# Kernel tuning notes

Hardware: AMD Instinct MI355X
Metric: run time of the kernel (lower is better)

## Reference

```python
import jax, jax.numpy as jnp
from jax import lax
import numpy as np

N_ATOMS, N_BONDS, N_GRAPHS = 8192, 32768, 256
EMBED, HIDDEN, DEPTH = 32, 256, 10
ATOM_VOCAB, BOND_VOCAB = 200, 10


def setup_inputs() -> dict:
    key = jax.random.key(0)
    ks = jax.random.split(key, 16)
    f = lambda k, *sh: jax.random.normal(k, sh, dtype=jnp.float32) * 0.05
    return {
        "atom_features": jax.random.randint(ks[0], (N_ATOMS,), 0, ATOM_VOCAB),
        "bond_features": jax.random.randint(ks[1], (N_BONDS,), 0, BOND_VOCAB),
        "adjacency_matrix": jax.random.randint(ks[2], (N_ATOMS, N_ATOMS), 0, 2, dtype=jnp.int32),
        "batch_indices": jax.random.randint(ks[3], (N_ATOMS,), 0, N_GRAPHS),
        "atom_emb": f(ks[4], ATOM_VOCAB, EMBED),
        "bond_emb": f(ks[5], BOND_VOCAB, EMBED),
        "msg_W": f(ks[6], DEPTH, HIDDEN, 2 * EMBED),
        "msg_b": f(ks[7], DEPTH, HIDDEN),
        "gru_Wih": f(ks[8], DEPTH, 3 * EMBED, HIDDEN),
        "gru_Whh": f(ks[9], DEPTH, 3 * EMBED, EMBED),
        "gru_bih": f(ks[10], DEPTH, 3 * EMBED),
        "gru_bhh": f(ks[11], DEPTH, 3 * EMBED),
        "pool_W": f(ks[12], HIDDEN, EMBED),
        "pool_b": f(ks[13], HIDDEN),
    }


def _gmpn(atom_emb, bond_emb, msg_W, msg_b, gru_Wih, gru_Whh, gru_bih, gru_bhh,
          pool_W, pool_b, atom_features, bond_features, adjacency_matrix, batch_indices):
    H = atom_emb[atom_features]                       # [N, E]
    A = (adjacency_matrix > 0).astype(H.dtype)        # [N, N] 0/1
    deg = A.sum(axis=1)                               # [N]
    has_nb = deg > 0
    inv_deg = jnp.where(has_nb, 1.0 / jnp.maximum(deg, 1.0), 0.0)[:, None]

    def layer(h, params):
        W, b, wih, whh, b_ih, b_hh = params
        # mean_j Linear([h_i ; h_j]) = W1 h_i + W2 mean_j h_j + b
        neigh_mean = (A @ h) * inv_deg                # [N, E]
        W1, W2 = W[:, :EMBED], W[:, EMBED:]
        msg = h @ W1.T + neigh_mean @ W2.T + b        # [N, HIDDEN]
        msg = jnp.where(has_nb[:, None], msg, 0.0)    # zero message if no neighbors
        # single-step GRU: input=msg, hidden state=h
        gi = msg @ wih.T + b_ih
        gh = h @ whh.T + b_hh
        ir, iz, inn = jnp.split(gi, 3, axis=-1)
        hr, hz, hn = jnp.split(gh, 3, axis=-1)
        r = jax.nn.sigmoid(ir + hr)
        z = jax.nn.sigmoid(iz + hz)
        n = jnp.tanh(inn + r * hn)
        h_new = (1.0 - z) * n + z * h                 # [N, E]
        return h_new, None

    H, _ = lax.scan(layer, H, (msg_W, msg_b, gru_Wih, gru_Whh, gru_bih, gru_bhh))

    # per-graph mean pooling (zeros for empty graphs), then global_pool linear
    seg_sum = jax.ops.segment_sum(H, batch_indices, num_segments=N_GRAPHS)
    cnt = jax.ops.segment_sum(jnp.ones((H.shape[0],), H.dtype), batch_indices, num_segments=N_GRAPHS)
    graph_mean = jnp.where(cnt[:, None] > 0, seg_sum / jnp.maximum(cnt, 1.0)[:, None], 0.0)
    graph_embeddings = graph_mean @ pool_W.T + pool_b  # [G, HIDDEN]

    bond_embeddings = bond_emb[bond_features]          # [B, E]
    return H, bond_embeddings, graph_embeddings


def reference(atom_features, bond_features, adjacency_matrix, batch_indices,
              atom_emb, bond_emb, msg_W, msg_b, gru_Wih, gru_Whh, gru_bih, gru_bhh,
              pool_W, pool_b):
    return _gmpn(atom_emb, bond_emb, msg_W, msg_b, gru_Wih, gru_Whh, gru_bih, gru_bhh,
                 pool_W, pool_b, atom_features, bond_features, adjacency_matrix, batch_indices)
```

## Files before the change

### kernel.cpp

```cpp
#include <hip/hip_runtime.h>
#include <stdint.h>

typedef __bf16 bf16x8 __attribute__((ext_vector_type(8)));
typedef float f32x4 __attribute__((ext_vector_type(4)));

__device__ __forceinline__ float b2f(unsigned short u){
  unsigned int t = ((unsigned int)u) << 16;
  return __builtin_bit_cast(float, t);
}
__device__ __forceinline__ unsigned short f2b(float f){
  unsigned int x = __builtin_bit_cast(unsigned int, f);
  x = x + 0x7FFFu + ((x >> 16) & 1u);
  return (unsigned short)(x >> 16);
}
__device__ __forceinline__ void spread8(unsigned int B, unsigned int w[4]){
  unsigned int m = __umul24(B, 0x8001u);
  w[0] = __umul24(m & 0x00010001u, 0x3F80u);
  w[1] = __umul24(m & 0x00040004u, 0x0FE0u);
  w[2] = __umul24(m & 0x00100010u, 0x03F8u);
  w[3] = __umul24(m & 0x00400040u, 0x00FEu);
}
__device__ __forceinline__ float fsig(float x){ return 1.f/(1.f + __expf(-x)); }
__device__ __forceinline__ float ftanh(float x){ return 1.f - 2.f/(__expf(2.f*x) + 1.f); }

__global__ void k_prep(const void* s_msgW, const void* s_msgb, const void* s_wih,
                       const void* s_whh, const void* s_bih, const void* s_bhh,
                       const void* s_poolW, const void* s_poolb,
                       const unsigned short* __restrict__ aemb_u16,
                       unsigned short* __restrict__ cw,
                       int* __restrict__ deg, float* __restrict__ seg,
                       float* __restrict__ cnt, int* __restrict__ flag){
  int b = blockIdx.x, t = threadIdx.x;
  unsigned int uu = aemb_u16[2*t];
  int e = (int)((uu >> 7) & 0xFF);
  unsigned long long vote = __ballot(e >= 100 && e <= 127);
  int isb = (__popcll(vote) > 32) ? 1 : 0;
  if (b < 1771){
    int id = b*256 + t;
    if (id < 453248){
      const void* src; int off;
      if      (id < 163840){ src = s_msgW;  off = id; }
      else if (id < 166400){ src = s_msgb;  off = id - 163840; }
      else if (id < 412160){ src = s_wih;   off = id - 166400; }
      else if (id < 442880){ src = s_whh;   off = id - 412160; }
      else if (id < 443840){ src = s_bih;   off = id - 442880; }
      else if (id < 444800){ src = s_bhh;   off = id - 443840; }
      else if (id < 452992){ src = s_poolW; off = id - 444800; }
      else                 { src = s_poolb; off = id - 452992; }
      cw[id] = isb ? ((const unsigned short*)src)[off]
                   : f2b(((const float*)src)[off]);
    }
  } else {
    int id2 = (b - 1771)*256 + t;
    if (id2 < 8192){ deg[id2] = 0; seg[id2] = 0.f; }
    if (id2 < 256) cnt[id2] = 0.f;
    if (b == 1771 && t == 0) flag[0] = isb;
  }
}

__global__ void k_pack(const int* __restrict__ adj, unsigned int* __restrict__ mask3,
                       int* __restrict__ deg){
  int tid = blockIdx.x*256 + threadIdx.x;
  int rb  = tid >> 12;
  int rem = tid & 4095;
  int kgg = rem >> 6;
  int L   = rem & 63;
  int lc = L & 15, q = L >> 4;
  int row = rb*16 + lc;
  const int4* p4 = (const int4*)(adj + (size_t)row*8192 + kgg*128 + q*8);
  unsigned int dw = 0; int pc = 0;
  #pragma unroll
  for (int s=0;s<4;s++){
    int4 u = p4[s*8];
    int4 v = p4[s*8 + 1];
    unsigned int b = (unsigned int)(u.x > 0)
                   | ((unsigned int)(u.y > 0) << 1)
                   | ((unsigned int)(u.z > 0) << 2)
                   | ((unsigned int)(u.w > 0) << 3)
                   | ((unsigned int)(v.x > 0) << 4)
                   | ((unsigned int)(v.y > 0) << 5)
                   | ((unsigned int)(v.z > 0) << 6)
                   | ((unsigned int)(v.w > 0) << 7);
    dw |= b << (8*s);
    pc += __popc(b);
  }
  mask3[tid] = dw;
  pc += __shfl_xor(pc, 16);
  pc += __shfl_xor(pc, 32);
  if (q == 0) atomicAdd(deg + row, pc);
}

__global__ void k_be(const int* __restrict__ af, const void* __restrict__ araw,
                     const int* __restrict__ bft, const void* __restrict__ braw,
                     const int* __restrict__ flag,
                     float* __restrict__ hf32, uint4* __restrict__ hfrag,
                     unsigned short* __restrict__ outB16, float* __restrict__ outB32){
  int b = blockIdx.x, t = threadIdx.x;
  if (b >= 512){
    int id = (b - 512)*512 + t;
    int e = id >> 5, c = id & 31;
    int idx = bft[e]*32 + c;
    if (flag[0]) outB16[id] = ((const unsigned short*)braw)[idx];
    else         outB32[id] = ((const float*)braw)[idx];
    return;
  }
  __shared__ __align__(16) float sh[512];
  int r = t >> 5, c = t & 31;
  int row = b*16 + r;
  int idx = af[row]*32 + c;
  float f;
  if (flag[0]) f = b2f(((const unsigned short*)araw)[idx]);
  else         f = ((const float*)araw)[idx];
  hf32[row*32 + c] = f;
  sh[r*32 + c] = f;
  __syncthreads();
  if (t < 64){
    int nt = t >> 5, Lq = t & 31;
    int ks32 = b >> 1, half = b & 1;
    int col = nt*16 + (Lq & 15);
    int rbase = (Lq >> 4)*8;
    unsigned int w[4];
    #pragma unroll
    for (int p=0;p<4;p++){
      unsigned int lo = f2b(sh[(rbase + 2*p    )*32 + col]);
      unsigned int hi = f2b(sh[(rbase + 2*p + 1)*32 + col]);
      w[p] = lo | (hi << 16);
    }
    hfrag[(ks32*2 + nt)*64 + half*32 + Lq] = make_uint4(w[0],w[1],w[2],w[3]);
  }
}

__launch_bounds__(512, 1)
__global__ void k_layer(const unsigned int* __restrict__ mask3,
                        const uint4* __restrict__ hfragIn,
                        unsigned int* __restrict__ hfragOut,
                        float* __restrict__ hf32,
                        const int* __restrict__ deg,
                        const unsigned short* __restrict__ msgW,
                        const unsigned short* __restrict__ msgb,
                        const unsigned short* __restrict__ wih,
                        const unsigned short* __restrict__ whh,
                        const unsigned short* __restrict__ bih,
                        const unsigned short* __restrict__ bhh,
                        const int* __restrict__ bidx,
                        float* __restrict__ seg, float* __restrict__ cnt,
                        unsigned short* __restrict__ out16, float* __restrict__ out32,
                        const int* __restrict__ flag, int last)
{
  __shared__ __align__(16) char uni[33792];
  __shared__ __align__(16) unsigned short sA[32][72];
  __shared__ __align__(16) unsigned short smsg[32][264];
  __shared__ int sdeg[32];

  const int t = threadIdx.x;
  const int b = blockIdx.x;
  const int w = t >> 6, L = t & 63;
  const int q = L >> 4, lc = L & 15;
  const int rowbase = b*32;

  const int r0 = t >> 4;
  const int cl = t & 15;
  const int r  = rowbase + r0;
  const int isb = flag[0];
  const int dgr = deg[r];
  const float invr = dgr > 0 ? 1.f/(float)dgr : 0.f;
  float h0 = hf32[r*32 + cl];
  float h1 = hf32[r*32 + 16 + cl];
  sA[r0][cl]    = f2b(h0);
  sA[r0][16+cl] = f2b(h1);
  if (cl == 0) sdeg[r0] = dgr;

  {
    f32x4 a00={0,0,0,0}, a01={0,0,0,0}, a10={0,0,0,0}, a11={0,0,0,0};
    const unsigned int* mp = mask3 + (size_t)b*8192 + w*512 + L;
    const uint4* bp = hfragIn + (size_t)w*4096 + L;
    for (int g=0; g<8; g++){
      unsigned int mw0 = mp[g*64];
      unsigned int mw1 = mp[4096 + g*64];
      #pragma unroll
      for (int s=0; s<4; s++){
        int ks = g*4 + s;
        uint4 u0 = bp[ks*128];
        uint4 u1 = bp[ks*128 + 64];
        union { unsigned int u[4]; bf16x8 v; } A0, A1, B0, B1;
        spread8((mw0 >> (8*s)) & 0xFFu, A0.u);
        spread8((mw1 >> (8*s)) & 0xFFu, A1.u);
        B0.u[0]=u0.x; B0.u[1]=u0.y; B0.u[2]=u0.z; B0.u[3]=u0.w;
        B1.u[0]=u1.x; B1.u[1]=u1.y; B1.u[2]=u1.z; B1.u[3]=u1.w;
        a00 = __builtin_amdgcn_mfma_f32_16x16x32_bf16(A0.v, B0.v, a00, 0,0,0);
        a01 = __builtin_amdgcn_mfma_f32_16x16x32_bf16(A0.v, B1.v, a01, 0,0,0);
        a10 = __builtin_amdgcn_mfma_f32_16x16x32_bf16(A1.v, B0.v, a10, 0,0,0);
        a11 = __builtin_amdgcn_mfma_f32_16x16x32_bf16(A1.v, B1.v, a11, 0,0,0);
      }
    }
    float* sp = (float*)uni + w*1056;
    #pragma unroll
    for (int rg=0; rg<4; rg++){
      int rw = q*4 + rg;
      sp[rw*33 + lc]         = a00[rg];
      sp[rw*33 + 16 + lc]    = a01[rg];
      sp[(16+rw)*33 + lc]    = a10[rg];
      sp[(16+rw)*33 + 16+lc] = a11[rg];
    }
  }
  __syncthreads();
  {
    const float* spf = (const float*)uni;
    float s0 = 0.f, s1 = 0.f;
    #pragma unroll
    for (int ww=0; ww<8; ww++){
      s0 += spf[ww*1056 + r0*33 + cl];
      s1 += spf[ww*1056 + r0*33 + 16 + cl];
    }
    sA[r0][32+cl] = f2b(s0*invr);
    sA[r0][48+cl] = f2b(s1*invr);
  }
  __syncthreads();
  {
    int rt = w & 1, ntb = (w >> 1)*4;
    union { uint4 u; bf16x8 v; } A0, A1;
    A0.u = *(const uint4*)&sA[rt*16 + lc][q*8];
    A1.u = *(const uint4*)&sA[rt*16 + lc][32 + q*8];
    #pragma unroll
    for (int i=0; i<4; i++){
      int nt = ntb + i;
      union { uint4 u; bf16x8 v; } B0, B1;
      B0.u = *(const uint4*)(msgW + (size_t)(nt*16 + lc)*64 + q*8);
      B1.u = *(const uint4*)(msgW + (size_t)(nt*16 + lc)*64 + 32 + q*8);
      f32x4 am = {0,0,0,0};
      am = __builtin_amdgcn_mfma_f32_16x16x32_bf16(A0.v, B0.v, am, 0,0,0);
      am = __builtin_amdgcn_mfma_f32_16x16x32_bf16(A1.v, B1.v, am, 0,0,0);
      float bv = b2f(msgb[nt*16 + lc]);
      #pragma unroll
      for (int rg=0; rg<4; rg++){
        int rw = rt*16 + q*4 + rg;
        float v = am[rg] + bv;
        if (sdeg[rw] == 0) v = 0.f;
        smsg[rw][nt*16 + lc] = f2b(v);
      }
    }
  }
  __syncthreads();
  {
    float* sgi = (float*)uni;
    float* sgh = (float*)(uni + 12800);
    if (w < 6){
      int nt = w;
      f32x4 g0 = {0,0,0,0}, g1 = {0,0,0,0};
      #pragma unroll
      for (int ks=0; ks<8; ks++){
        union { uint4 u; bf16x8 v; } A0, A1, B;
        B.u  = *(const uint4*)(wih + (size_t)(nt*16 + lc)*256 + ks*32 + q*8);
        A0.u = *(const uint4*)&smsg[lc][ks*32 + q*8];
        A1.u = *(const uint4*)&smsg[16 + lc][ks*32 + q*8];
        g0 = __builtin_amdgcn_mfma_f32_16x16x32_bf16(A0.v, B.v, g0, 0,0,0);
        g1 = __builtin_amdgcn_mfma_f32_16x16x32_bf16(A1.v, B.v, g1, 0,0,0);
      }
      #pragma unroll
      for (int rg=0; rg<4; rg++){
        sgi[(q*4+rg)*100      + nt*16 + lc] = g0[rg];
        sgi[(16+q*4+rg)*100   + nt*16 + lc] = g1[rg];
      }
    } else {
      int rt = w - 6;
      union { uint4 u; bf16x8 v; } A;
      A.u = *(const uint4*)&sA[rt*16 + lc][q*8];
      #pragma unroll
      for (int nt=0; nt<6; nt++){
        union { uint4 u; bf16x8 v; } B;
        B.u = *(const uint4*)(whh + (size_t)(nt*16 + lc)*32 + q*8);
        f32x4 hh = {0,0,0,0};
        hh = __builtin_amdgcn_mfma_f32_16x16x32_bf16(A.v, B.v, hh, 0,0,0);
        #pragma unroll
        for (int rg=0; rg<4; rg++)
          sgh[(rt*16 + q*4+rg)*100 + nt*16 + lc] = hh[rg];
      }
    }
  }
  __syncthreads();
  {
    const float* sgi = (const float*)uni;
    const float* sgh = (const float*)(uni + 12800);
    float ir0 = sgi[r0*100 + cl]    + b2f(bih[cl]),    hr0 = sgh[r0*100 + cl]    + b2f(bhh[cl]);
    float iz0 = sgi[r0*100 + 32+cl] + b2f(bih[32+cl]), hz0 = sgh[r0*100 + 32+cl] + b2f(bhh[32+cl]);
    float in0 = sgi[r0*100 + 64+cl] + b2f(bih[64+cl]), hn0 = sgh[r0*100 + 64+cl] + b2f(bhh[64+cl]);
    float ir1 = sgi[r0*100 + 16+cl] + b2f(bih[16+cl]), hr1 = sgh[r0*100 + 16+cl] + b2f(bhh[16+cl]);
    float iz1 = sgi[r0*100 + 48+cl] + b2f(bih[48+cl]), hz1 = sgh[r0*100 + 48+cl] + b2f(bhh[48+cl]);
    float in1 = sgi[r0*100 + 80+cl] + b2f(bih[80+cl]), hn1 = sgh[r0*100 + 80+cl] + b2f(bhh[80+cl]);
    float rr0 = fsig(ir0 + hr0), zz0 = fsig(iz0 + hz0);
    float rr1 = fsig(ir1 + hr1), zz1 = fsig(iz1 + hz1);
    float nn0 = ftanh(in0 + rr0*hn0);
    float nn1 = ftanh(in1 + rr1*hn1);
    h0 = (1.f - zz0)*nn0 + zz0*h0;
    h1 = (1.f - zz1)*nn1 + zz1*h1;
    hf32[r*32 + cl]      = h0;
    hf32[r*32 + 16 + cl] = h1;
    unsigned int m0 = f2b(h0), m1 = f2b(h1);
    if (!last){
      unsigned int p0 = (unsigned int)__shfl_xor((int)m0, 16);
      unsigned int p1 = (unsigned int)__shfl_xor((int)m1, 16);
      if ((r & 1) == 0){
        int ks32 = r >> 5;
        int Lf = ((r >> 3) & 3)*16 + cl;
        int pidx = (r & 7) >> 1;
        hfragOut[((ks32*2 + 0)*64 + Lf)*4 + pidx] = m0 | (p0 << 16);
        hfragOut[((ks32*2 + 1)*64 + Lf)*4 + pidx] = m1 | (p1 << 16);
      }
    } else {
      if (isb){ out16[r*32 + cl] = (unsigned short)m0; out16[r*32 + 16 + cl] = (unsigned short)m1; }
      else    { out32[r*32 + cl] = h0; out32[r*32 + 16 + cl] = h1; }
      int gb = bidx[r];
      atomicAdd(seg + gb*32 + cl, h0);
      atomicAdd(seg + gb*32 + 16 + cl, h1);
      if (cl == 0) atomicAdd(cnt + gb, 1.f);
    }
  }
}

__global__ void k_pool(const float* __restrict__ seg, const float* __restrict__ cnt,
                       const unsigned short* __restrict__ pw, const unsigned short* __restrict__ pb,
                       const int* __restrict__ flag,
                       unsigned short* __restrict__ outG16, float* __restrict__ outG32){
  int g = blockIdx.x, o = threadIdx.x;
  float cv = cnt[g];
  float ic = cv > 0.f ? 1.f/cv : 0.f;
  float s = 0.f;
  #pragma unroll
  for (int c=0;c<32;c++) s += seg[g*32+c]*ic*b2f(pw[o*32+c]);
  s += b2f(pb[o]);
  if (flag[0]) outG16[g*256 + o] = f2b(s);
  else         outG32[g*256 + o] = s;
}

extern "C" void kernel_launch(void* const* d_in, const int* in_sizes, int n_in,
                              void* d_out, int out_size, void* d_ws, size_t ws_size,
                              hipStream_t stream){
  const int* af   = (const int*)d_in[0];
  const int* bft  = (const int*)d_in[1];
  const int* adj  = (const int*)d_in[2];
  const int* bidx = (const int*)d_in[3];

  char* ws = (char*)d_ws;
  unsigned int*   mask3  = (unsigned int*)(ws + 0);
  unsigned int*   hfrag0 = (unsigned int*)(ws + 8388608);
  unsigned int*   hfrag1 = (unsigned int*)(ws + 8912896);
  float*          hf32   = (float*)(ws + 9437184);
  int*            deg    = (int*)(ws + 10485760);
  float*          seg    = (float*)(ws + 10518528);
  float*          cnt    = (float*)(ws + 10551296);
  int*            flag   = (int*)(ws + 10552320);
  unsigned short* cw     = (unsigned short*)(ws + 10552384);

  unsigned short* o16 = (unsigned short*)d_out;
  float*          o32 = (float*)d_out;

  k_prep<<<1803, 256, 0, stream>>>(d_in[6], d_in[7], d_in[8], d_in[9], d_in[10],
                                   d_in[11], d_in[12], d_in[13],
                                   (const unsigned short*)d_in[4],
                                   cw, deg, seg, cnt, flag);
  k_pack<<<8192, 256, 0, stream>>>(adj, mask3, deg);
  k_be<<<2560, 512, 0, stream>>>(af, d_in[4], bft, d_in[5], flag,
                                 hf32, (uint4*)hfrag0,
                                 o16 + 262144, o32 + 262144);

  for (int d = 0; d < 10; d++){
    const uint4*  hin  = (const uint4*)((d & 1) ? hfrag1 : hfrag0);
    unsigned int* hout = (d & 1) ? hfrag0 : hfrag1;
    k_layer<<<256, 512, 0, stream>>>(mask3, hin, hout, hf32, deg,
                                     cw + (size_t)d*16384,        cw + 163840 + d*256,
                                     cw + 166400 + (size_t)d*24576, cw + 412160 + d*3072,
                                     cw + 442880 + d*96,          cw + 443840 + d*96,
                                     bidx, seg, cnt, o16, o32, flag, (d == 9) ? 1 : 0);
  }
  k_pool<<<256, 256, 0, stream>>>(seg, cnt, cw + 444800, cw + 452992, flag,
                                  o16 + 1310720, o32 + 1310720);
}
```

Before: 535.5 us.

## Precompose message and GRU input weights to skip the hidden-256 message matmul

```diff
diff --git a/kernel.cpp b/kernel.cpp
--- a/kernel.cpp
+++ b/kernel.cpp
@@ -58,6 +58,32 @@
   }
 }
 
+__global__ void k_fuse(const unsigned short* __restrict__ cw,
+                       unsigned short* __restrict__ vcat, float* __restrict__ bwv){
+  int d = blockIdx.x >> 2, quarter = blockIdx.x & 3;
+  const unsigned short* msgW = cw + (size_t)d*16384;
+  const unsigned short* msgb = cw + 163840 + d*256;
+  const unsigned short* wih  = cw + 166400 + (size_t)d*24576;
+  int t = threadIdx.x;
+  #pragma unroll
+  for (int i=0;i<6;i++){
+    int idx = quarter*1536 + i*256 + t;
+    int j = idx >> 6, e = idx & 63;
+    const unsigned short* wr = wih + j*256;
+    const unsigned short* wc = msgW + e;
+    float acc = 0.f;
+    for (int k=0;k<256;k++)
+      acc += b2f(wr[k]) * b2f(wc[k*64]);
+    vcat[(size_t)d*6144 + idx] = f2b(acc);
+  }
+  if (quarter == 0 && t < 96){
+    const unsigned short* wr = wih + t*256;
+    float acc = 0.f;
+    for (int k=0;k<256;k++) acc += b2f(msgb[k]) * b2f(wr[k]);
+    bwv[d*96 + t] = acc;
+  }
+}
+
 __global__ void k_pack(const int* __restrict__ adj, unsigned int* __restrict__ mask3,
                        int* __restrict__ deg){
   int tid = blockIdx.x*256 + threadIdx.x;
@@ -136,9 +162,8 @@
                         unsigned int* __restrict__ hfragOut,
                         float* __restrict__ hf32,
                         const int* __restrict__ deg,
-                        const unsigned short* __restrict__ msgW,
-                        const unsigned short* __restrict__ msgb,
-                        const unsigned short* __restrict__ wih,
+                        const unsigned short* __restrict__ vcat,
+                        const float* __restrict__ bwv,
                         const unsigned short* __restrict__ whh,
                         const unsigned short* __restrict__ bih,
                         const unsigned short* __restrict__ bhh,
@@ -149,7 +174,6 @@
 {
   __shared__ __align__(16) char uni[33792];
   __shared__ __align__(16) unsigned short sA[32][72];
-  __shared__ __align__(16) unsigned short smsg[32][264];
   __shared__ int sdeg[32];
 
   const int t = threadIdx.x;
@@ -217,49 +241,29 @@
   }
   __syncthreads();
   {
-    int rt = w & 1, ntb = (w >> 1)*4;
-    union { uint4 u; bf16x8 v; } A0, A1;
-    A0.u = *(const uint4*)&sA[rt*16 + lc][q*8];
-    A1.u = *(const uint4*)&sA[rt*16 + lc][32 + q*8];
-    #pragma unroll
-    for (int i=0; i<4; i++){
-      int nt = ntb + i;
-      union { uint4 u; bf16x8 v; } B0, B1;
-      B0.u = *(const uint4*)(msgW + (size_t)(nt*16 + lc)*64 + q*8);
-      B1.u = *(const uint4*)(msgW + (size_t)(nt*16 + lc)*64 + 32 + q*8);
-      f32x4 am = {0,0,0,0};
-      am = __builtin_amdgcn_mfma_f32_16x16x32_bf16(A0.v, B0.v, am, 0,0,0);
-      am = __builtin_amdgcn_mfma_f32_16x16x32_bf16(A1.v, B1.v, am, 0,0,0);
-      float bv = b2f(msgb[nt*16 + lc]);
-      #pragma unroll
-      for (int rg=0; rg<4; rg++){
-        int rw = rt*16 + q*4 + rg;
-        float v = am[rg] + bv;
-        if (sdeg[rw] == 0) v = 0.f;
-        smsg[rw][nt*16 + lc] = f2b(v);
-      }
-    }
-  }
-  __syncthreads();
-  {
     float* sgi = (float*)uni;
     float* sgh = (float*)(uni + 12800);
     if (w < 6){
       int nt = w;
-      f32x4 g0 = {0,0,0,0}, g1 = {0,0,0,0};
+      union { uint4 u; bf16x8 v; } B0, B1;
+      B0.u = *(const uint4*)(vcat + (size_t)(nt*16 + lc)*64 + q*8);
+      B1.u = *(const uint4*)(vcat + (size_t)(nt*16 + lc)*64 + 32 + q*8);
+      float bw = bwv[nt*16 + lc];
       #pragma unroll
-      for (int ks=0; ks<8; ks++){
-        union { uint4 u; bf16x8 v; } A0, A1, B;
-        B.u  = *(const uint4*)(wih + (size_t)(nt*16 + lc)*256 + ks*32 + q*8);
-        A0.u = *(const uint4*)&smsg[lc][ks*32 + q*8];
-        A1.u = *(const uint4*)&smsg[16 + lc][ks*32 + q*8];
-        g0 = __builtin_amdgcn_mfma_f32_16x16x32_bf16(A0.v, B.v, g0, 0,0,0);
-        g1 = __builtin_amdgcn_mfma_f32_16x16x32_bf16(A1.v, B.v, g1, 0,0,0);
-      }
-      #pragma unroll
-      for (int rg=0; rg<4; rg++){
-        sgi[(q*4+rg)*100      + nt*16 + lc] = g0[rg];
-        sgi[(16+q*4+rg)*100   + nt*16 + lc] = g1[rg];
+      for (int rt=0; rt<2; rt++){
+        union { uint4 u; bf16x8 v; } A0, A1;
+        A0.u = *(const uint4*)&sA[rt*16 + lc][q*8];
+        A1.u = *(const uint4*)&sA[rt*16 + lc][32 + q*8];
+        f32x4 g0 = {0,0,0,0};
+        g0 = __builtin_amdgcn_mfma_f32_16x16x32_bf16(A0.v, B0.v, g0, 0,0,0);
+        g0 = __builtin_amdgcn_mfma_f32_16x16x32_bf16(A1.v, B1.v, g0, 0,0,0);
+        #pragma unroll
+        for (int rg=0; rg<4; rg++){
+          int rw = rt*16 + q*4 + rg;
+          float v = g0[rg] + bw;
+          if (sdeg[rw] == 0) v = 0.f;
+          sgi[rw*100 + nt*16 + lc] = v;
+        }
       }
     } else {
       int rt = w - 6;
@@ -350,6 +354,8 @@
   float*          cnt    = (float*)(ws + 10551296);
   int*            flag   = (int*)(ws + 10552320);
   unsigned short* cw     = (unsigned short*)(ws + 10552384);
+  unsigned short* vcat   = (unsigned short*)(ws + 11458880);
+  float*          bwv    = (float*)(ws + 11581760);
 
   unsigned short* o16 = (unsigned short*)d_out;
   float*          o32 = (float*)d_out;
@@ -358,6 +364,7 @@
                                    d_in[11], d_in[12], d_in[13],
                                    (const unsigned short*)d_in[4],
                                    cw, deg, seg, cnt, flag);
+  k_fuse<<<40, 256, 0, stream>>>(cw, vcat, bwv);
   k_pack<<<8192, 256, 0, stream>>>(adj, mask3, deg);
   k_be<<<2560, 512, 0, stream>>>(af, d_in[4], bft, d_in[5], flag,
                                  hf32, (uint4*)hfrag0,
@@ -367,9 +374,9 @@
     const uint4*  hin  = (const uint4*)((d & 1) ? hfrag1 : hfrag0);
     unsigned int* hout = (d & 1) ? hfrag0 : hfrag1;
     k_layer<<<256, 512, 0, stream>>>(mask3, hin, hout, hf32, deg,
-                                     cw + (size_t)d*16384,        cw + 163840 + d*256,
-                                     cw + 166400 + (size_t)d*24576, cw + 412160 + d*3072,
-                                     cw + 442880 + d*96,          cw + 443840 + d*96,
+                                     vcat + (size_t)d*6144, bwv + d*96,
+                                     cw + 412160 + d*3072,
+                                     cw + 442880 + d*96, cw + 443840 + d*96,
                                      bidx, seg, cnt, o16, o32, flag, (d == 9) ? 1 : 0);
   }
   k_pool<<<256, 256, 0, stream>>>(seg, cnt, cw + 444800, cw + 452992, flag,
```

After: 550.0 us. +2.7%, slower.

## Fuse ten layer launches into one persistent kernel with grid barrier

Applied to the files above, without the earlier changes.

```diff
diff --git a/kernel.cpp b/kernel.cpp
--- a/kernel.cpp
+++ b/kernel.cpp
@@ -22,6 +22,25 @@
 }
 __device__ __forceinline__ float fsig(float x){ return 1.f/(1.f + __expf(-x)); }
 __device__ __forceinline__ float ftanh(float x){ return 1.f - 2.f/(__expf(2.f*x) + 1.f); }
+
+__device__ __forceinline__ void gbar(int* bar){
+  __syncthreads();
+  if (threadIdx.x == 0){
+    int g = __hip_atomic_load(&bar[1], __ATOMIC_RELAXED, __HIP_MEMORY_SCOPE_AGENT);
+    int a = __hip_atomic_fetch_add(&bar[0], 1, __ATOMIC_RELEASE, __HIP_MEMORY_SCOPE_AGENT);
+    if (a == 255){
+      __hip_atomic_store(&bar[0], 0, __ATOMIC_RELAXED, __HIP_MEMORY_SCOPE_AGENT);
+      __hip_atomic_fetch_add(&bar[1], 1, __ATOMIC_RELEASE, __HIP_MEMORY_SCOPE_AGENT);
+    } else {
+      int it = 0;
+      while (__hip_atomic_load(&bar[1], __ATOMIC_RELAXED, __HIP_MEMORY_SCOPE_AGENT) == g){
+        if (++it > 48) __builtin_amdgcn_s_sleep(1);
+      }
+    }
+    (void)__hip_atomic_load(&bar[1], __ATOMIC_ACQUIRE, __HIP_MEMORY_SCOPE_AGENT);
+  }
+  __syncthreads();
+}
 
 __global__ void k_prep(const void* s_msgW, const void* s_msgb, const void* s_wih,
                        const void* s_whh, const void* s_bih, const void* s_bhh,
@@ -54,7 +73,7 @@
     int id2 = (b - 1771)*256 + t;
     if (id2 < 8192){ deg[id2] = 0; seg[id2] = 0.f; }
     if (id2 < 256) cnt[id2] = 0.f;
-    if (b == 1771 && t == 0) flag[0] = isb;
+    if (b == 1771 && t == 0){ flag[0] = isb; flag[4] = 0; flag[5] = 0; }
   }
 }
 
@@ -130,22 +149,17 @@
   }
 }
 
-__launch_bounds__(512, 1)
-__global__ void k_layer(const unsigned int* __restrict__ mask3,
-                        const uint4* __restrict__ hfragIn,
-                        unsigned int* __restrict__ hfragOut,
-                        float* __restrict__ hf32,
-                        const int* __restrict__ deg,
-                        const unsigned short* __restrict__ msgW,
-                        const unsigned short* __restrict__ msgb,
-                        const unsigned short* __restrict__ wih,
-                        const unsigned short* __restrict__ whh,
-                        const unsigned short* __restrict__ bih,
-                        const unsigned short* __restrict__ bhh,
-                        const int* __restrict__ bidx,
-                        float* __restrict__ seg, float* __restrict__ cnt,
-                        unsigned short* __restrict__ out16, float* __restrict__ out32,
-                        const int* __restrict__ flag, int last)
+__launch_bounds__(512)
+__global__ void k_layers(const unsigned int* __restrict__ mask3,
+                         unsigned int* __restrict__ hfrag0,
+                         unsigned int* __restrict__ hfrag1,
+                         const float* __restrict__ hf32,
+                         const int* __restrict__ deg,
+                         const unsigned short* __restrict__ cw,
+                         const int* __restrict__ bidx,
+                         float* __restrict__ seg, float* __restrict__ cnt,
+                         unsigned short* __restrict__ out16, float* __restrict__ out32,
+                         const int* __restrict__ flag, int* bar)
 {
   __shared__ __align__(16) char uni[33792];
   __shared__ __align__(16) unsigned short sA[32][72];
@@ -166,154 +180,166 @@
   const float invr = dgr > 0 ? 1.f/(float)dgr : 0.f;
   float h0 = hf32[r*32 + cl];
   float h1 = hf32[r*32 + 16 + cl];
-  sA[r0][cl]    = f2b(h0);
-  sA[r0][16+cl] = f2b(h1);
   if (cl == 0) sdeg[r0] = dgr;
 
-  {
-    f32x4 a00={0,0,0,0}, a01={0,0,0,0}, a10={0,0,0,0}, a11={0,0,0,0};
-    const unsigned int* mp = mask3 + (size_t)b*8192 + w*512 + L;
-    const uint4* bp = hfragIn + (size_t)w*4096 + L;
-    for (int g=0; g<8; g++){
-      unsigned int mw0 = mp[g*64];
-      unsigned int mw1 = mp[4096 + g*64];
-      #pragma unroll
-      for (int s=0; s<4; s++){
-        int ks = g*4 + s;
-        uint4 u0 = bp[ks*128];
-        uint4 u1 = bp[ks*128 + 64];
-        union { unsigned int u[4]; bf16x8 v; } A0, A1, B0, B1;
-        spread8((mw0 >> (8*s)) & 0xFFu, A0.u);
-        spread8((mw1 >> (8*s)) & 0xFFu, A1.u);
-        B0.u[0]=u0.x; B0.u[1]=u0.y; B0.u[2]=u0.z; B0.u[3]=u0.w;
-        B1.u[0]=u1.x; B1.u[1]=u1.y; B1.u[2]=u1.z; B1.u[3]=u1.w;
-        a00 = __builtin_amdgcn_mfma_f32_16x16x32_bf16(A0.v, B0.v, a00, 0,0,0);
-        a01 = __builtin_amdgcn_mfma_f32_16x16x32_bf16(A0.v, B1.v, a01, 0,0,0);
-        a10 = __builtin_amdgcn_mfma_f32_16x16x32_bf16(A1.v, B0.v, a10, 0,0,0);
-        a11 = __builtin_amdgcn_mfma_f32_16x16x32_bf16(A1.v, B1.v, a11, 0,0,0);
-      }
-    }
-    float* sp = (float*)uni + w*1056;
-    #pragma unroll
-    for (int rg=0; rg<4; rg++){
-      int rw = q*4 + rg;
-      sp[rw*33 + lc]         = a00[rg];
-      sp[rw*33 + 16 + lc]    = a01[rg];
-      sp[(16+rw)*33 + lc]    = a10[rg];
-      sp[(16+rw)*33 + 16+lc] = a11[rg];
-    }
-  }
-  __syncthreads();
-  {
-    const float* spf = (const float*)uni;
-    float s0 = 0.f, s1 = 0.f;
-    #pragma unroll
-    for (int ww=0; ww<8; ww++){
-      s0 += spf[ww*1056 + r0*33 + cl];
-      s1 += spf[ww*1056 + r0*33 + 16 + cl];
-    }
-    sA[r0][32+cl] = f2b(s0*invr);
-    sA[r0][48+cl] = f2b(s1*invr);
-  }
-  __syncthreads();
-  {
-    int rt = w & 1, ntb = (w >> 1)*4;
-    union { uint4 u; bf16x8 v; } A0, A1;
-    A0.u = *(const uint4*)&sA[rt*16 + lc][q*8];
-    A1.u = *(const uint4*)&sA[rt*16 + lc][32 + q*8];
-    #pragma unroll
-    for (int i=0; i<4; i++){
-      int nt = ntb + i;
-      union { uint4 u; bf16x8 v; } B0, B1;
-      B0.u = *(const uint4*)(msgW + (size_t)(nt*16 + lc)*64 + q*8);
-      B1.u = *(const uint4*)(msgW + (size_t)(nt*16 + lc)*64 + 32 + q*8);
-      f32x4 am = {0,0,0,0};
-      am = __builtin_amdgcn_mfma_f32_16x16x32_bf16(A0.v, B0.v, am, 0,0,0);
-      am = __builtin_amdgcn_mfma_f32_16x16x32_bf16(A1.v, B1.v, am, 0,0,0);
-      float bv = b2f(msgb[nt*16 + lc]);
+  for (int d = 0; d < 10; ++d){
+    const unsigned short* msgW = cw + (size_t)d*16384;
+    const unsigned short* msgb = cw + 163840 + d*256;
+    const unsigned short* wih  = cw + 166400 + (size_t)d*24576;
+    const unsigned short* whh  = cw + 412160 + d*3072;
+    const unsigned short* bih  = cw + 442880 + d*96;
+    const unsigned short* bhh  = cw + 443840 + d*96;
+    const uint4*  hfragIn  = (const uint4*)((d & 1) ? hfrag1 : hfrag0);
+    unsigned int* hfragOut = (d & 1) ? hfrag0 : hfrag1;
+    const int last = (d == 9);
+
+    sA[r0][cl]    = f2b(h0);
+    sA[r0][16+cl] = f2b(h1);
+
+    {
+      f32x4 a00={0,0,0,0}, a01={0,0,0,0}, a10={0,0,0,0}, a11={0,0,0,0};
+      const unsigned int* mp = mask3 + (size_t)b*8192 + w*512 + L;
+      const uint4* bp = hfragIn + (size_t)w*4096 + L;
+      for (int g=0; g<8; g++){
+        unsigned int mw0 = mp[g*64];
+        unsigned int mw1 = mp[4096 + g*64];
+        #pragma unroll
+        for (int s=0; s<4; s++){
+          int ks = g*4 + s;
+          uint4 u0 = bp[ks*128];
+          uint4 u1 = bp[ks*128 + 64];
+          union { unsigned int u[4]; bf16x8 v; } A0, A1, B0, B1;
+          spread8((mw0 >> (8*s)) & 0xFFu, A0.u);
+          spread8((mw1 >> (8*s)) & 0xFFu, A1.u);
+          B0.u[0]=u0.x; B0.u[1]=u0.y; B0.u[2]=u0.z; B0.u[3]=u0.w;
+          B1.u[0]=u1.x; B1.u[1]=u1.y; B1.u[2]=u1.z; B1.u[3]=u1.w;
+          a00 = __builtin_amdgcn_mfma_f32_16x16x32_bf16(A0.v, B0.v, a00, 0,0,0);
+          a01 = __builtin_amdgcn_mfma_f32_16x16x32_bf16(A0.v, B1.v, a01, 0,0,0);
+          a10 = __builtin_amdgcn_mfma_f32_16x16x32_bf16(A1.v, B0.v, a10, 0,0,0);
+          a11 = __builtin_amdgcn_mfma_f32_16x16x32_bf16(A1.v, B1.v, a11, 0,0,0);
+        }
+      }
+      float* sp = (float*)uni + w*1056;
       #pragma unroll
       for (int rg=0; rg<4; rg++){
-        int rw = rt*16 + q*4 + rg;
-        float v = am[rg] + bv;
-        if (sdeg[rw] == 0) v = 0.f;
-        smsg[rw][nt*16 + lc] = f2b(v);
-      }
-    }
-  }
-  __syncthreads();
-  {
-    float* sgi = (float*)uni;
-    float* sgh = (float*)(uni + 12800);
-    if (w < 6){
-      int nt = w;
-      f32x4 g0 = {0,0,0,0}, g1 = {0,0,0,0};
+        int rw = q*4 + rg;
+        sp[rw*33 + lc]         = a00[rg];
+        sp[rw*33 + 16 + lc]    = a01[rg];
+        sp[(16+rw)*33 + lc]    = a10[rg];
+        sp[(16+rw)*33 + 16+lc] = a11[rg];
+      }
+    }
+    __syncthreads();
+    {
+      const float* spf = (const float*)uni;
+      float s0 = 0.f, s1 = 0.f;
       #pragma unroll
-      for (int ks=0; ks<8; ks++){
-        union { uint4 u; bf16x8 v; } A0, A1, B;
-        B.u  = *(const uint4*)(wih + (size_t)(nt*16 + lc)*256 + ks*32 + q*8);
-        A0.u = *(const uint4*)&smsg[lc][ks*32 + q*8];
-        A1.u = *(const uint4*)&smsg[16 + lc][ks*32 + q*8];
-        g0 = __builtin_amdgcn_mfma_f32_16x16x32_bf16(A0.v, B.v, g0, 0,0,0);
-        g1 = __builtin_amdgcn_mfma_f32_16x16x32_bf16(A1.v, B.v, g1, 0,0,0);
-      }
+      for (int ww=0; ww<8; ww++){
+        s0 += spf[ww*1056 + r0*33 + cl];
+        s1 += spf[ww*1056 + r0*33 + 16 + cl];
+      }
+      sA[r0][32+cl] = f2b(s0*invr);
+      sA[r0][48+cl] = f2b(s1*invr);
+    }
+    __syncthreads();
+    {
+      int rt = w & 1, ntb = (w >> 1)*4;
+      union { uint4 u; bf16x8 v; } A0, A1;
+      A0.u = *(const uint4*)&sA[rt*16 + lc][q*8];
+      A1.u = *(const uint4*)&sA[rt*16 + lc][32 + q*8];
       #pragma unroll
-      for (int rg=0; rg<4; rg++){
-        sgi[(q*4+rg)*100      + nt*16 + lc] = g0[rg];
-        sgi[(16+q*4+rg)*100   + nt*16 + lc] = g1[rg];
-      }
-    } else {
-      int rt = w - 6;
-      union { uint4 u; bf16x8 v; } A;
-      A.u = *(const uint4*)&sA[rt*16 + lc][q*8];
-      #pragma unroll
-      for (int nt=0; nt<6; nt++){
-        union { uint4 u; bf16x8 v; } B;
-        B.u = *(const uint4*)(whh + (size_t)(nt*16 + lc)*32 + q*8);
-        f32x4 hh = {0,0,0,0};
-        hh = __builtin_amdgcn_mfma_f32_16x16x32_bf16(A.v, B.v, hh, 0,0,0);
-        #pragma unroll
-        for (int rg=0; rg<4; rg++)
-          sgh[(rt*16 + q*4+rg)*100 + nt*16 + lc] = hh[rg];
-      }
-    }
-  }
-  __syncthreads();
-  {
-    const float* sgi = (const float*)uni;
-    const float* sgh = (const float*)(uni + 12800);
-    float ir0 = sgi[r0*100 + cl]    + b2f(bih[cl]),    hr0 = sgh[r0*100 + cl]    + b2f(bhh[cl]);
-    float iz0 = sgi[r0*100 + 32+cl] + b2f(bih[32+cl]), hz0 = sgh[r0*100 + 32+cl] + b2f(bhh[32+cl]);
-    float in0 = sgi[r0*100 + 64+cl] + b2f(bih[64+cl]), hn0 = sgh[r0*100 + 64+cl] + b2f(bhh[64+cl]);
-    float ir1 = sgi[r0*100 + 16+cl] + b2f(bih[16+cl]), hr1 = sgh[r0*100 + 16+cl] + b2f(bhh[16+cl]);
-    float iz1 = sgi[r0*100 + 48+cl] + b2f(bih[48+cl]), hz1 = sgh[r0*100 + 48+cl] + b2f(bhh[48+cl]);
-    float in1 = sgi[r0*100 + 80+cl] + b2f(bih[80+cl]), hn1 = sgh[r0*100 + 80+cl] + b2f(bhh[80+cl]);
-    float rr0 = fsig(ir0 + hr0), zz0 = fsig(iz0 + hz0);
-    float rr1 = fsig(ir1 + hr1), zz1 = fsig(iz1 + hz1);
-    float nn0 = ftanh(in0 + rr0*hn0);
-    float nn1 = ftanh(in1 + rr1*hn1);
-    h0 = (1.f - zz0)*nn0 + zz0*h0;
-    h1 = (1.f - zz1)*nn1 + zz1*h1;
-    hf32[r*32 + cl]      = h0;
-    hf32[r*32 + 16 + cl] = h1;
-    unsigned int m0 = f2b(h0), m1 = f2b(h1);
-    if (!last){
-      unsigned int p0 = (unsigned int)__shfl_xor((int)m0, 16);
-      unsigned int p1 = (unsigned int)__shfl_xor((int)m1, 16);
-      if ((r & 1) == 0){
-        int ks32 = r >> 5;
-        int Lf = ((r >> 3) & 3)*16 + cl;
-        int pidx = (r & 7) >> 1;
-        hfragOut[((ks32*2 + 0)*64 + Lf)*4 + pidx] = m0 | (p0 << 16);
-        hfragOut[((ks32*2 + 1)*64 + Lf)*4 + pidx] = m1 | (p1 << 16);
-      }
-    } else {
-      if (isb){ out16[r*32 + cl] = (unsigned short)m0; out16[r*32 + 16 + cl] = (unsigned short)m1; }
-      else    { out32[r*32 + cl] = h0; out32[r*32 + 16 + cl] = h1; }
-      int gb = bidx[r];
-      atomicAdd(seg + gb*32 + cl, h0);
-      atomicAdd(seg + gb*32 + 16 + cl, h1);
-      if (cl == 0) atomicAdd(cnt + gb, 1.f);
-    }
+      for (int i=0; i<4; i++){
+        int nt = ntb + i;
+        union { uint4 u; bf16x8 v; } B0, B1;
+        B0.u = *(const uint4*)(msgW + (size_t)(nt*16 + lc)*64 + q*8);
+        B1.u = *(const uint4*)(msgW + (size_t)(nt*16 + lc)*64 + 32 + q*8);
+        f32x4 am = {0,0,0,0};
+        am = __builtin_amdgcn_mfma_f32_16x16x32_bf16(A0.v, B0.v, am, 0,0,0);
+        am = __builtin_amdgcn_mfma_f32_16x16x32_bf16(A1.v, B1.v, am, 0,0,0);
+        float bv = b2f(msgb[nt*16 + lc]);
+        #pragma unroll
+        for (int rg=0; rg<4; rg++){
+          int rw = rt*16 + q*4 + rg;
+          float v = am[rg] + bv;
+          if (sdeg[rw] == 0) v = 0.f;
+          smsg[rw][nt*16 + lc] = f2b(v);
+        }
+      }
+    }
+    __syncthreads();
+    {
+      float* sgi = (float*)uni;
+      float* sgh = (float*)(uni + 12800);
+      if (w < 6){
+        int nt = w;
+        f32x4 g0 = {0,0,0,0}, g1 = {0,0,0,0};
+        #pragma unroll
+        for (int ks=0; ks<8; ks++){
+          union { uint4 u; bf16x8 v; } A0, A1, B;
+          B.u  = *(const uint4*)(wih + (size_t)(nt*16 + lc)*256 + ks*32 + q*8);
+          A0.u = *(const uint4*)&smsg[lc][ks*32 + q*8];
+          A1.u = *(const uint4*)&smsg[16 + lc][ks*32 + q*8];
+          g0 = __builtin_amdgcn_mfma_f32_16x16x32_bf16(A0.v, B.v, g0, 0,0,0);
+          g1 = __builtin_amdgcn_mfma_f32_16x16x32_bf16(A1.v, B.v, g1, 0,0,0);
+        }
+        #pragma unroll
+        for (int rg=0; rg<4; rg++){
+          sgi[(q*4+rg)*100      + nt*16 + lc] = g0[rg];
+          sgi[(16+q*4+rg)*100   + nt*16 + lc] = g1[rg];
+        }
+      } else {
+        int rt = w - 6;
+        union { uint4 u; bf16x8 v; } A;
+        A.u = *(const uint4*)&sA[rt*16 + lc][q*8];
+        #pragma unroll
+        for (int nt=0; nt<6; nt++){
+          union { uint4 u; bf16x8 v; } B;
+          B.u = *(const uint4*)(whh + (size_t)(nt*16 + lc)*32 + q*8);
+          f32x4 hh = {0,0,0,0};
+          hh = __builtin_amdgcn_mfma_f32_16x16x32_bf16(A.v, B.v, hh, 0,0,0);
+          #pragma unroll
+          for (int rg=0; rg<4; rg++)
+            sgh[(rt*16 + q*4+rg)*100 + nt*16 + lc] = hh[rg];
+        }
+      }
+    }
+    __syncthreads();
+    {
+      const float* sgi = (const float*)uni;
+      const float* sgh = (const float*)(uni + 12800);
+      float ir0 = sgi[r0*100 + cl]    + b2f(bih[cl]),    hr0 = sgh[r0*100 + cl]    + b2f(bhh[cl]);
+      float iz0 = sgi[r0*100 + 32+cl] + b2f(bih[32+cl]), hz0 = sgh[r0*100 + 32+cl] + b2f(bhh[32+cl]);
+      float in0 = sgi[r0*100 + 64+cl] + b2f(bih[64+cl]), hn0 = sgh[r0*100 + 64+cl] + b2f(bhh[64+cl]);
+      float ir1 = sgi[r0*100 + 16+cl] + b2f(bih[16+cl]), hr1 = sgh[r0*100 + 16+cl] + b2f(bhh[16+cl]);
+      float iz1 = sgi[r0*100 + 48+cl] + b2f(bih[48+cl]), hz1 = sgh[r0*100 + 48+cl] + b2f(bhh[48+cl]);
+      float in1 = sgi[r0*100 + 80+cl] + b2f(bih[80+cl]), hn1 = sgh[r0*100 + 80+cl] + b2f(bhh[80+cl]);
+      float rr0 = fsig(ir0 + hr0), zz0 = fsig(iz0 + hz0);
+      float rr1 = fsig(ir1 + hr1), zz1 = fsig(iz1 + hz1);
+      float nn0 = ftanh(in0 + rr0*hn0);
+      float nn1 = ftanh(in1 + rr1*hn1);
+      h0 = (1.f - zz0)*nn0 + zz0*h0;
+      h1 = (1.f - zz1)*nn1 + zz1*h1;
+      unsigned int m0 = f2b(h0), m1 = f2b(h1);
+      if (!last){
+        unsigned int p0 = (unsigned int)__shfl_xor((int)m0, 16);
+        unsigned int p1 = (unsigned int)__shfl_xor((int)m1, 16);
+        if ((r & 1) == 0){
+          int ks32 = r >> 5;
+          int Lf = ((r >> 3) & 3)*16 + cl;
+          int pidx = (r & 7) >> 1;
+          hfragOut[((ks32*2 + 0)*64 + Lf)*4 + pidx] = m0 | (p0 << 16);
+          hfragOut[((ks32*2 + 1)*64 + Lf)*4 + pidx] = m1 | (p1 << 16);
+        }
+      } else {
+        if (isb){ out16[r*32 + cl] = (unsigned short)m0; out16[r*32 + 16 + cl] = (unsigned short)m1; }
+        else    { out32[r*32 + cl] = h0; out32[r*32 + 16 + cl] = h1; }
+        int gb = bidx[r];
+        atomicAdd(seg + gb*32 + cl, h0);
+        atomicAdd(seg + gb*32 + 16 + cl, h1);
+        if (cl == 0) atomicAdd(cnt + gb, 1.f);
+      }
+    }
+    if (!last) gbar(bar);
   }
 }
 
@@ -353,6 +379,7 @@
 
   unsigned short* o16 = (unsigned short*)d_out;
   float*          o32 = (float*)d_out;
+  int*            bar = flag + 4;
 
   k_prep<<<1803, 256, 0, stream>>>(d_in[6], d_in[7], d_in[8], d_in[9], d_in[10],
                                    d_in[11], d_in[12], d_in[13],
@@ -363,15 +390,9 @@
                                  hf32, (uint4*)hfrag0,
                                  o16 + 262144, o32 + 262144);
 
-  for (int d = 0; d < 10; d++){
-    const uint4*  hin  = (const uint4*)((d & 1) ? hfrag1 : hfrag0);
-    unsigned int* hout = (d & 1) ? hfrag0 : hfrag1;
-    k_layer<<<256, 512, 0, stream>>>(mask3, hin, hout, hf32, deg,
-                                     cw + (size_t)d*16384,        cw + 163840 + d*256,
-                                     cw + 166400 + (size_t)d*24576, cw + 412160 + d*3072,
-                                     cw + 442880 + d*96,          cw + 443840 + d*96,
-                                     bidx, seg, cnt, o16, o32, flag, (d == 9) ? 1 : 0);
-  }
+  k_layers<<<256, 512, 0, stream>>>(mask3, hfrag0, hfrag1, hf32, deg, cw,
+                                    bidx, seg, cnt, o16, o32, flag, bar);
+
   k_pool<<<256, 256, 0, stream>>>(seg, cnt, cw + 444800, cw + 452992, flag,
                                   o16 + 1310720, o32 + 1310720);
 }
```

Measured after the change: 632.0 us. 18.0% more time.

## Fuse adjacency bit-packing into first layer kernel and merge setup kernels

Applied to the files above, without the earlier changes.

```diff
diff --git a/kernel.cpp b/kernel.cpp
--- a/kernel.cpp
+++ b/kernel.cpp
@@ -23,20 +23,25 @@
 __device__ __forceinline__ float fsig(float x){ return 1.f/(1.f + __expf(-x)); }
 __device__ __forceinline__ float ftanh(float x){ return 1.f - 2.f/(__expf(2.f*x) + 1.f); }
 
-__global__ void k_prep(const void* s_msgW, const void* s_msgb, const void* s_wih,
-                       const void* s_whh, const void* s_bih, const void* s_bhh,
-                       const void* s_poolW, const void* s_poolb,
-                       const unsigned short* __restrict__ aemb_u16,
-                       unsigned short* __restrict__ cw,
-                       int* __restrict__ deg, float* __restrict__ seg,
-                       float* __restrict__ cnt, int* __restrict__ flag){
+__global__ void k_setup(const void* s_msgW, const void* s_msgb, const void* s_wih,
+                        const void* s_whh, const void* s_bih, const void* s_bhh,
+                        const void* s_poolW, const void* s_poolb,
+                        const unsigned short* __restrict__ aemb_u16,
+                        const int* __restrict__ af, const void* __restrict__ araw,
+                        const int* __restrict__ bft, const void* __restrict__ braw,
+                        unsigned short* __restrict__ cw,
+                        float* __restrict__ seg, float* __restrict__ cnt,
+                        int* __restrict__ flag,
+                        float* __restrict__ hf32, uint4* __restrict__ hfrag,
+                        unsigned short* __restrict__ outB16, float* __restrict__ outB32){
   int b = blockIdx.x, t = threadIdx.x;
   unsigned int uu = aemb_u16[2*t];
   int e = (int)((uu >> 7) & 0xFF);
   unsigned long long vote = __ballot(e >= 100 && e <= 127);
   int isb = (__popcll(vote) > 32) ? 1 : 0;
-  if (b < 1771){
-    int id = b*256 + t;
+
+  if (b < 886){
+    int id = b*512 + t;
     if (id < 453248){
       const void* src; int off;
       if      (id < 163840){ src = s_msgW;  off = id; }
@@ -50,92 +55,60 @@
       cw[id] = isb ? ((const unsigned short*)src)[off]
                    : f2b(((const float*)src)[off]);
     }
-  } else {
-    int id2 = (b - 1771)*256 + t;
-    if (id2 < 8192){ deg[id2] = 0; seg[id2] = 0.f; }
-    if (id2 < 256) cnt[id2] = 0.f;
-    if (b == 1771 && t == 0) flag[0] = isb;
-  }
-}
-
-__global__ void k_pack(const int* __restrict__ adj, unsigned int* __restrict__ mask3,
-                       int* __restrict__ deg){
-  int tid = blockIdx.x*256 + threadIdx.x;
-  int rb  = tid >> 12;
-  int rem = tid & 4095;
-  int kgg = rem >> 6;
-  int L   = rem & 63;
-  int lc = L & 15, q = L >> 4;
-  int row = rb*16 + lc;
-  const int4* p4 = (const int4*)(adj + (size_t)row*8192 + kgg*128 + q*8);
-  unsigned int dw = 0; int pc = 0;
-  #pragma unroll
-  for (int s=0;s<4;s++){
-    int4 u = p4[s*8];
-    int4 v = p4[s*8 + 1];
-    unsigned int b = (unsigned int)(u.x > 0)
-                   | ((unsigned int)(u.y > 0) << 1)
-                   | ((unsigned int)(u.z > 0) << 2)
-                   | ((unsigned int)(u.w > 0) << 3)
-                   | ((unsigned int)(v.x > 0) << 4)
-                   | ((unsigned int)(v.y > 0) << 5)
-                   | ((unsigned int)(v.z > 0) << 6)
-                   | ((unsigned int)(v.w > 0) << 7);
-    dw |= b << (8*s);
-    pc += __popc(b);
-  }
-  mask3[tid] = dw;
-  pc += __shfl_xor(pc, 16);
-  pc += __shfl_xor(pc, 32);
-  if (q == 0) atomicAdd(deg + row, pc);
-}
-
-__global__ void k_be(const int* __restrict__ af, const void* __restrict__ araw,
-                     const int* __restrict__ bft, const void* __restrict__ braw,
-                     const int* __restrict__ flag,
-                     float* __restrict__ hf32, uint4* __restrict__ hfrag,
-                     unsigned short* __restrict__ outB16, float* __restrict__ outB32){
-  int b = blockIdx.x, t = threadIdx.x;
-  if (b >= 512){
-    int id = (b - 512)*512 + t;
-    int e = id >> 5, c = id & 31;
-    int idx = bft[e]*32 + c;
-    if (flag[0]) outB16[id] = ((const unsigned short*)braw)[idx];
-    else         outB32[id] = ((const float*)braw)[idx];
     return;
   }
-  __shared__ __align__(16) float sh[512];
-  int r = t >> 5, c = t & 31;
-  int row = b*16 + r;
-  int idx = af[row]*32 + c;
-  float f;
-  if (flag[0]) f = b2f(((const unsigned short*)araw)[idx]);
-  else         f = ((const float*)araw)[idx];
-  hf32[row*32 + c] = f;
-  sh[r*32 + c] = f;
-  __syncthreads();
-  if (t < 64){
-    int nt = t >> 5, Lq = t & 31;
-    int ks32 = b >> 1, half = b & 1;
-    int col = nt*16 + (Lq & 15);
-    int rbase = (Lq >> 4)*8;
-    unsigned int w[4];
+  if (b == 886){
     #pragma unroll
-    for (int p=0;p<4;p++){
-      unsigned int lo = f2b(sh[(rbase + 2*p    )*32 + col]);
-      unsigned int hi = f2b(sh[(rbase + 2*p + 1)*32 + col]);
-      w[p] = lo | (hi << 16);
-    }
-    hfrag[(ks32*2 + nt)*64 + half*32 + Lq] = make_uint4(w[0],w[1],w[2],w[3]);
-  }
-}
-
+    for (int i=0;i<16;i++){ int j = i*512 + t; seg[j] = 0.f; }
+    if (t < 256) cnt[t] = 0.f;
+    if (t == 0) flag[0] = isb;
+    return;
+  }
+  if (b < 1399){
+    __shared__ __align__(16) float sh[512];
+    int eb = b - 887;
+    int r = t >> 5, c = t & 31;
+    int row = eb*16 + r;
+    int idx = af[row]*32 + c;
+    float f;
+    if (isb) f = b2f(((const unsigned short*)araw)[idx]);
+    else     f = ((const float*)araw)[idx];
+    hf32[row*32 + c] = f;
+    sh[r*32 + c] = f;
+    __syncthreads();
+    if (t < 64){
+      int nt = t >> 5, Lq = t & 31;
+      int ks32 = eb >> 1, half = eb & 1;
+      int col = nt*16 + (Lq & 15);
+      int rbase = (Lq >> 4)*8;
+      unsigned int w[4];
+      #pragma unroll
+      for (int p=0;p<4;p++){
+        unsigned int lo = f2b(sh[(rbase + 2*p    )*32 + col]);
+        unsigned int hi = f2b(sh[(rbase + 2*p + 1)*32 + col]);
+        w[p] = lo | (hi << 16);
+      }
+      hfrag[(ks32*2 + nt)*64 + half*32 + Lq] = make_uint4(w[0],w[1],w[2],w[3]);
+    }
+    return;
+  }
+  {
+    int id = (b - 1399)*512 + t;
+    int e2 = id >> 5, c = id & 31;
+    int idx = bft[e2]*32 + c;
+    if (isb) outB16[id] = ((const unsigned short*)braw)[idx];
+    else     outB32[id] = ((const float*)braw)[idx];
+  }
+}
+
+template<int FIRST>
 __launch_bounds__(512, 1)
-__global__ void k_layer(const unsigned int* __restrict__ mask3,
+__global__ void k_layer(const int* __restrict__ adj,
+                        unsigned int* __restrict__ mask3,
                         const uint4* __restrict__ hfragIn,
                         unsigned int* __restrict__ hfragOut,
                         float* __restrict__ hf32,
-                        const int* __restrict__ deg,
+                        int* __restrict__ deg,
                         const unsigned short* __restrict__ msgW,
                         const unsigned short* __restrict__ msgb,
                         const unsigned short* __restrict__ wih,
@@ -150,6 +123,7 @@
   __shared__ __align__(16) char uni[33792];
   __shared__ __align__(16) unsigned short sA[32][72];
   __shared__ __align__(16) unsigned short smsg[32][264];
+  __shared__ __align__(16) unsigned int smask[FIRST ? 8192 : 64];
   __shared__ int sdeg[32];
 
   const int t = threadIdx.x;
@@ -162,35 +136,98 @@
   const int cl = t & 15;
   const int r  = rowbase + r0;
   const int isb = flag[0];
-  const int dgr = deg[r];
-  const float invr = dgr > 0 ? 1.f/(float)dgr : 0.f;
   float h0 = hf32[r*32 + cl];
   float h1 = hf32[r*32 + 16 + cl];
   sA[r0][cl]    = f2b(h0);
   sA[r0][16+cl] = f2b(h1);
-  if (cl == 0) sdeg[r0] = dgr;
+
+  if (FIRST){
+    if (t < 32) sdeg[t] = 0;
+    __syncthreads();
+    #pragma unroll
+    for (int i=0;i<16;i++){
+      int l = i*512 + t;
+      int rbl = l >> 12;
+      int rem = l & 4095;
+      int kgg = rem >> 6;
+      int L2  = rem & 63;
+      int lc2 = L2 & 15, q2 = L2 >> 4;
+      int row = rowbase + rbl*16 + lc2;
+      const int4* p4 = (const int4*)(adj + (size_t)row*8192 + kgg*128 + q2*8);
+      unsigned int dw = 0; int pc = 0;
+      #pragma unroll
+      for (int s2=0;s2<4;s2++){
+        int4 u = p4[s2*8];
+        int4 v = p4[s2*8 + 1];
+        unsigned int bb = (unsigned int)(u.x > 0)
+                        | ((unsigned int)(u.y > 0) << 1)
+                        | ((unsigned int)(u.z > 0) << 2)
+                        | ((unsigned int)(u.w > 0) << 3)
+                        | ((unsigned int)(v.x > 0) << 4)
+                        | ((unsigned int)(v.y > 0) << 5)
+                        | ((unsigned int)(v.z > 0) << 6)
+                        | ((unsigned int)(v.w > 0) << 7);
+        dw |= bb << (8*s2);
+        pc += __popc(bb);
+      }
+      smask[l] = dw;
+      mask3[(size_t)b*8192 + l] = dw;
+      pc += __shfl_xor(pc, 16);
+      pc += __shfl_xor(pc, 32);
+      if (q2 == 0) atomicAdd(&sdeg[rbl*16 + lc2], pc);
+    }
+    __syncthreads();
+    if (t < 32) deg[rowbase + t] = sdeg[t];
+  }
+
+  const int dgr = FIRST ? sdeg[r0] : deg[r];
+  if (!FIRST && cl == 0) sdeg[r0] = dgr;
+  const float invr = dgr > 0 ? 1.f/(float)dgr : 0.f;
 
   {
     f32x4 a00={0,0,0,0}, a01={0,0,0,0}, a10={0,0,0,0}, a11={0,0,0,0};
-    const unsigned int* mp = mask3 + (size_t)b*8192 + w*512 + L;
     const uint4* bp = hfragIn + (size_t)w*4096 + L;
-    for (int g=0; g<8; g++){
-      unsigned int mw0 = mp[g*64];
-      unsigned int mw1 = mp[4096 + g*64];
-      #pragma unroll
-      for (int s=0; s<4; s++){
-        int ks = g*4 + s;
-        uint4 u0 = bp[ks*128];
-        uint4 u1 = bp[ks*128 + 64];
-        union { unsigned int u[4]; bf16x8 v; } A0, A1, B0, B1;
-        spread8((mw0 >> (8*s)) & 0xFFu, A0.u);
-        spread8((mw1 >> (8*s)) & 0xFFu, A1.u);
-        B0.u[0]=u0.x; B0.u[1]=u0.y; B0.u[2]=u0.z; B0.u[3]=u0.w;
-        B1.u[0]=u1.x; B1.u[1]=u1.y; B1.u[2]=u1.z; B1.u[3]=u1.w;
-        a00 = __builtin_amdgcn_mfma_f32_16x16x32_bf16(A0.v, B0.v, a00, 0,0,0);
-        a01 = __builtin_amdgcn_mfma_f32_16x16x32_bf16(A0.v, B1.v, a01, 0,0,0);
-        a10 = __builtin_amdgcn_mfma_f32_16x16x32_bf16(A1.v, B0.v, a10, 0,0,0);
-        a11 = __builtin_amdgcn_mfma_f32_16x16x32_bf16(A1.v, B1.v, a11, 0,0,0);
+    if (FIRST){
+      const unsigned int* mp = smask + w*512 + L;
+      for (int g=0; g<8; g++){
+        unsigned int mw0 = mp[g*64];
+        unsigned int mw1 = mp[4096 + g*64];
+        #pragma unroll
+        for (int s=0; s<4; s++){
+          int ks = g*4 + s;
+          uint4 u0 = bp[ks*128];
+          uint4 u1 = bp[ks*128 + 64];
+          union { unsigned int u[4]; bf16x8 v; } A0, A1, B0, B1;
+          spread8((mw0 >> (8*s)) & 0xFFu, A0.u);
+          spread8((mw1 >> (8*s)) & 0xFFu, A1.u);
+          B0.u[0]=u0.x; B0.u[1]=u0.y; B0.u[2]=u0.z; B0.u[3]=u0.w;
+          B1.u[0]=u1.x; B1.u[1]=u1.y; B1.u[2]=u1.z; B1.u[3]=u1.w;
+          a00 = __builtin_amdgcn_mfma_f32_16x16x32_bf16(A0.v, B0.v, a00, 0,0,0);
+          a01 = __builtin_amdgcn_mfma_f32_16x16x32_bf16(A0.v, B1.v, a01, 0,0,0);
+          a10 = __builtin_amdgcn_mfma_f32_16x16x32_bf16(A1.v, B0.v, a10, 0,0,0);
+          a11 = __builtin_amdgcn_mfma_f32_16x16x32_bf16(A1.v, B1.v, a11, 0,0,0);
+        }
+      }
+    } else {
+      const unsigned int* mp = mask3 + (size_t)b*8192 + w*512 + L;
+      for (int g=0; g<8; g++){
+        unsigned int mw0 = mp[g*64];
+        unsigned int mw1 = mp[4096 + g*64];
+        #pragma unroll
+        for (int s=0; s<4; s++){
+          int ks = g*4 + s;
+          uint4 u0 = bp[ks*128];
+          uint4 u1 = bp[ks*128 + 64];
+          union { unsigned int u[4]; bf16x8 v; } A0, A1, B0, B1;
+          spread8((mw0 >> (8*s)) & 0xFFu, A0.u);
+          spread8((mw1 >> (8*s)) & 0xFFu, A1.u);
+          B0.u[0]=u0.x; B0.u[1]=u0.y; B0.u[2]=u0.z; B0.u[3]=u0.w;
+          B1.u[0]=u1.x; B1.u[1]=u1.y; B1.u[2]=u1.z; B1.u[3]=u1.w;
+          a00 = __builtin_amdgcn_mfma_f32_16x16x32_bf16(A0.v, B0.v, a00, 0,0,0);
+          a01 = __builtin_amdgcn_mfma_f32_16x16x32_bf16(A0.v, B1.v, a01, 0,0,0);
+          a10 = __builtin_amdgcn_mfma_f32_16x16x32_bf16(A1.v, B0.v, a10, 0,0,0);
+          a11 = __builtin_amdgcn_mfma_f32_16x16x32_bf16(A1.v, B1.v, a11, 0,0,0);
+        }
       }
     }
     float* sp = (float*)uni + w*1056;
@@ -354,23 +391,28 @@
   unsigned short* o16 = (unsigned short*)d_out;
   float*          o32 = (float*)d_out;
 
-  k_prep<<<1803, 256, 0, stream>>>(d_in[6], d_in[7], d_in[8], d_in[9], d_in[10],
-                                   d_in[11], d_in[12], d_in[13],
-                                   (const unsigned short*)d_in[4],
-                                   cw, deg, seg, cnt, flag);
-  k_pack<<<8192, 256, 0, stream>>>(adj, mask3, deg);
-  k_be<<<2560, 512, 0, stream>>>(af, d_in[4], bft, d_in[5], flag,
-                                 hf32, (uint4*)hfrag0,
-                                 o16 + 262144, o32 + 262144);
+  k_setup<<<3447, 512, 0, stream>>>(d_in[6], d_in[7], d_in[8], d_in[9], d_in[10],
+                                    d_in[11], d_in[12], d_in[13],
+                                    (const unsigned short*)d_in[4],
+                                    af, d_in[4], bft, d_in[5],
+                                    cw, seg, cnt, flag, hf32, (uint4*)hfrag0,
+                                    o16 + 262144, o32 + 262144);
 
   for (int d = 0; d < 10; d++){
     const uint4*  hin  = (const uint4*)((d & 1) ? hfrag1 : hfrag0);
     unsigned int* hout = (d & 1) ? hfrag0 : hfrag1;
-    k_layer<<<256, 512, 0, stream>>>(mask3, hin, hout, hf32, deg,
-                                     cw + (size_t)d*16384,        cw + 163840 + d*256,
-                                     cw + 166400 + (size_t)d*24576, cw + 412160 + d*3072,
-                                     cw + 442880 + d*96,          cw + 443840 + d*96,
-                                     bidx, seg, cnt, o16, o32, flag, (d == 9) ? 1 : 0);
+    if (d == 0)
+      k_layer<1><<<256, 512, 0, stream>>>(adj, mask3, hin, hout, hf32, deg,
+                                          cw + (size_t)d*16384,        cw + 163840 + d*256,
+                                          cw + 166400 + (size_t)d*24576, cw + 412160 + d*3072,
+                                          cw + 442880 + d*96,          cw + 443840 + d*96,
+                                          bidx, seg, cnt, o16, o32, flag, 0);
+    else
+      k_layer<0><<<256, 512, 0, stream>>>(adj, mask3, hin, hout, hf32, deg,
+                                          cw + (size_t)d*16384,        cw + 163840 + d*256,
+                                          cw + 166400 + (size_t)d*24576, cw + 412160 + d*3072,
+                                          cw + 442880 + d*96,          cw + 443840 + d*96,
+                                          bidx, seg, cnt, o16, o32, flag, (d == 9) ? 1 : 0);
   }
   k_pool<<<256, 256, 0, stream>>>(seg, cnt, cw + 444800, cw + 452992, flag,
                                   o16 + 1310720, o32 + 1310720);
```

Result: no change. 543.6 us (+1.5%).
